# Kernel optimization log

Hardware: AMD Instinct MI355X
Metric: run time of the kernel (lower is better)

## Reference

```python
import jax, jax.numpy as jnp
import numpy as np

D_MODEL = 1024
NUM_HEADS = 16
D_K = D_MODEL // NUM_HEADS
NEG_INF = -1e9


def setup_inputs() -> dict:
    key = jax.random.key(0)
    ks = jax.random.split(key, 12)
    B, S = 2, 2048
    scale = 1.0 / np.sqrt(D_MODEL)
    inp = {
        "q": jax.random.normal(ks[0], (B, S, D_MODEL), jnp.float32),
        "k": jax.random.normal(ks[1], (B, S, D_MODEL), jnp.float32),
        "v": jax.random.normal(ks[2], (B, S, D_MODEL), jnp.float32),
        "mask": jnp.ones((B, S), jnp.int32),
        "W_q": jax.random.normal(ks[3], (D_MODEL, D_MODEL), jnp.float32) * scale,
        "b_q": jnp.zeros((D_MODEL,), jnp.float32),
        "W_k": jax.random.normal(ks[4], (D_MODEL, D_MODEL), jnp.float32) * scale,
        "b_k": jnp.zeros((D_MODEL,), jnp.float32),
        "W_v": jax.random.normal(ks[5], (D_MODEL, D_MODEL), jnp.float32) * scale,
        "b_v": jnp.zeros((D_MODEL,), jnp.float32),
        "W_o": jax.random.normal(ks[6], (D_MODEL, D_MODEL), jnp.float32) * scale,
        "b_o": jnp.zeros((D_MODEL,), jnp.float32),
    }
    return inp


def reference(q, k, v, mask, W_q, b_q, W_k, b_k, W_v, b_v, W_o, b_o):
    B, S, _ = q.shape
    def proj(x, W, b):
        # [B,S,D] -> [B,H,S,d_k]
        y = x @ W.T + b
        return y.reshape(B, -1, NUM_HEADS, D_K).transpose(0, 2, 1, 3)
    qh = proj(q, W_q, b_q)
    kh = proj(k, W_k, b_k)
    vh = proj(v, W_v, b_v)
    scores = jnp.einsum("bhqd,bhkd->bhqk", qh, kh) / jnp.sqrt(jnp.float32(D_K))
    # 2D mask [B,S_k] -> broadcast over heads and query positions
    m = mask[:, None, None, :]
    scores = jnp.where(m == 0, jnp.float32(NEG_INF), scores)
    attn = jax.nn.softmax(scores, axis=-1)
    # dropout is identity at inference
    context = jnp.einsum("bhqk,bhkd->bhqd", attn, vh)
    context = context.transpose(0, 2, 1, 3).reshape(B, S, D_MODEL)
    return context @ W_o.T + b_o
```

## Files before the change

kernel.cpp:

```cpp
#include <hip/hip_runtime.h>
#include <hip/hip_bf16.h>
#include <cstdint>
#include <cstddef>

#define DMODEL 1024
#define NHEADS 16
#define DK 64
#define SEQ 2048
#define BATCH 2
#define NT2 (SEQ / 64)

typedef short bf16x8 __attribute__((ext_vector_type(8)));
typedef float f32x4 __attribute__((ext_vector_type(4)));
typedef float f32x16 __attribute__((ext_vector_type(16)));
typedef unsigned int u32x2 __attribute__((ext_vector_type(2)));
typedef unsigned int u32x4 __attribute__((ext_vector_type(4)));

typedef const __attribute__((address_space(1))) void* gas_ptr;
typedef __attribute__((address_space(3))) void* las_ptr;

__device__ __forceinline__ void gld_lds16(const void* g, void* l) {
    __builtin_amdgcn_global_load_lds((gas_ptr)g, (las_ptr)l, 16, 0, 0);
}

__device__ __forceinline__ ushort f2bf_u(float f) {
    uint32_t x = __float_as_uint(f);
    x += 0x7fff + ((x >> 16) & 1);
    return (ushort)(x >> 16);
}

__global__ __launch_bounds__(256) void cast_all(
        const float* __restrict__ q, const float* __restrict__ k,
        const float* __restrict__ v, const float* __restrict__ Wq,
        const float* __restrict__ Wk, const float* __restrict__ Wv,
        const float* __restrict__ Wo,
        ushort* __restrict__ qb, ushort* __restrict__ kb, ushort* __restrict__ vb,
        ushort* __restrict__ Wqb, ushort* __restrict__ Wkb,
        ushort* __restrict__ Wvb, ushort* __restrict__ Wob) {
    int bid = blockIdx.x;
    const float* src; ushort* dst; int base;
    if      (bid <  4096) { src = q;  dst = qb;  base = bid; }
    else if (bid <  8192) { src = k;  dst = kb;  base = bid - 4096; }
    else if (bid < 12288) { src = v;  dst = vb;  base = bid - 8192; }
    else if (bid < 13312) { src = Wq; dst = Wqb; base = bid - 12288; }
    else if (bid < 14336) { src = Wk; dst = Wkb; base = bid - 13312; }
    else if (bid < 15360) { src = Wv; dst = Wvb; base = bid - 14336; }
    else                  { src = Wo; dst = Wob; base = bid - 15360; }
    int i = base * 1024 + threadIdx.x * 4;
    float4 f = *reinterpret_cast<const float4*>(src + i);
    ushort4 o;
    o.x = f2bf_u(f.x); o.y = f2bf_u(f.y); o.z = f2bf_u(f.z); o.w = f2bf_u(f.w);
    *reinterpret_cast<ushort4*>(dst + i) = o;
}

__global__ __launch_bounds__(256) void mask2bias(
        const int* __restrict__ m, float* __restrict__ mb) {
    int i = (blockIdx.x * 256 + threadIdx.x) * 4;
    int4 mk = *reinterpret_cast<const int4*>(m + i);
    float4 o;
    o.x = mk.x ? 0.f : -1e9f;
    o.y = mk.y ? 0.f : -1e9f;
    o.z = mk.z ? 0.f : -1e9f;
    o.w = mk.w ? 0.f : -1e9f;
    *reinterpret_cast<float4*>(mb + i) = o;
}

__global__ __launch_bounds__(256) void gemm_qkv(
        const ushort* __restrict__ A,
        const ushort* __restrict__ Wall,
        const float* __restrict__ bq, const float* __restrict__ bk,
        const float* __restrict__ bv,
        ushort* __restrict__ Qh, ushort* __restrict__ Kh, ushort* __restrict__ Vt) {
    __shared__ ushort As[128 * 32];
    __shared__ ushort Bs[128 * 32];
    const int tid = threadIdx.x;
    const int w = tid >> 6, lane = tid & 63;
    const int lr = lane & 15, lg = lane >> 4;
    int lid = (blockIdx.x & 7) * 96 + (blockIdx.x >> 3);
    const int tMg = (lid >> 3) << 7;
    const int tN  = (lid & 7) << 7;
    const int g   = tMg >> 12;
    const ushort* W = Wall + (size_t)g * 1024 * 1024;
    const float* bias = (g == 0) ? bq : (g == 1 ? bk : bv);
    const int wr = (w >> 1) * 64, wc = (w & 1) * 64;

    f32x4 acc[4][4] = {};

    const int c0 = (w * 2 + 0) * 64 + lane;
    const int c1 = (w * 2 + 1) * 64 + lane;
    const ushort* gA0 = A + (size_t)(tMg + (c0 >> 2)) * 1024 + (c0 & 3) * 8;
    const ushort* gA1 = A + (size_t)(tMg + (c1 >> 2)) * 1024 + (c1 & 3) * 8;
    const ushort* gB0 = W + (size_t)(tN + (c0 >> 2)) * 1024 + (c0 & 3) * 8;
    const ushort* gB1 = W + (size_t)(tN + (c1 >> 2)) * 1024 + (c1 & 3) * 8;
    ushort* lA0 = As + (w * 2 + 0) * 512;
    ushort* lA1 = As + (w * 2 + 1) * 512;
    ushort* lB0 = Bs + (w * 2 + 0) * 512;
    ushort* lB1 = Bs + (w * 2 + 1) * 512;

    for (int k0 = 0; k0 < 1024; k0 += 32) {
        gld_lds16(gA0 + k0, lA0);
        gld_lds16(gA1 + k0, lA1);
        gld_lds16(gB0 + k0, lB0);
        gld_lds16(gB1 + k0, lB1);
        __syncthreads();

        bf16x8 af[4], bfr[4];
#pragma unroll
        for (int i = 0; i < 4; i++)
            af[i] = *(const bf16x8*)(As + (wr + i * 16 + lr) * 32 + lg * 8);
#pragma unroll
        for (int i = 0; i < 4; i++)
            bfr[i] = *(const bf16x8*)(Bs + (wc + i * 16 + lr) * 32 + lg * 8);
#pragma unroll
        for (int mi = 0; mi < 4; mi++)
#pragma unroll
            for (int ni = 0; ni < 4; ni++)
                acc[mi][ni] = __builtin_amdgcn_mfma_f32_16x16x32_bf16(
                    af[mi], bfr[ni], acc[mi][ni], 0, 0, 0);
        __syncthreads();
    }

#pragma unroll
    for (int mi = 0; mi < 4; mi++) {
        const int row0 = tMg + wr + mi * 16 + lg * 4;
#pragma unroll
        for (int ni = 0; ni < 4; ni++) {
            const int col = tN + wc + ni * 16 + lr;
            const int h = col >> 6, d = col & (DK - 1);
            const float bvv = bias[col];
            if (g == 2) {
                int mloc = row0 & 4095;
                int b = mloc >> 11, s0 = mloc & (SEQ - 1);
                ushort4 o4;
                o4.x = f2bf_u(acc[mi][ni][0] + bvv);
                o4.y = f2bf_u(acc[mi][ni][1] + bvv);
                o4.z = f2bf_u(acc[mi][ni][2] + bvv);
                o4.w = f2bf_u(acc[mi][ni][3] + bvv);
                *reinterpret_cast<ushort4*>(
                    &Vt[(((size_t)(b * NHEADS + h) * DK + d) * SEQ) + s0]) = o4;
            } else {
#pragma unroll
                for (int r = 0; r < 4; r++) {
                    float vv = acc[mi][ni][r] + bvv;
                    int mloc = (row0 + r) & 4095;
                    int b = mloc >> 11, s = mloc & (SEQ - 1);
                    if (g == 0)
                        Qh[(((size_t)(b * NHEADS + h) * SEQ + s) * DK) + d] = f2bf_u(vv);
                    else
                        Kh[(((size_t)(b * NHEADS + h) * SEQ + s) * DK) + d] = f2bf_u(vv);
                }
            }
        }
    }
}

__global__ __launch_bounds__(256) void gemm_out(
        const ushort* __restrict__ A,
        const ushort* __restrict__ W,
        const float* __restrict__ bias,
        float* __restrict__ out, int M, int N, int K) {
    __shared__ ushort As[64 * 32];
    __shared__ ushort Bs[128 * 32];
    const int tid = threadIdx.x;
    const int w = tid >> 6, lane = tid & 63;
    const int lr = lane & 15, lg = lane >> 4;
    const int nTiles = N >> 7;
    const int cpx = gridDim.x >> 3;
    int lid = (blockIdx.x & 7) * cpx + (blockIdx.x >> 3);
    const int tM = (lid / nTiles) << 6;
    const int tN = (lid % nTiles) << 7;
    const int wr = (w >> 1) * 32, wc = (w & 1) * 64;

    f32x4 acc[2][4] = {};

    const int cA = w * 64 + lane;
    const int cB0 = w * 128 + lane;
    const int cB1 = w * 128 + 64 + lane;
    const ushort* gA  = A + (size_t)(tM + (cA  >> 2)) * K + (cA  & 3) * 8;
    const ushort* gB0 = W + (size_t)(tN + (cB0 >> 2)) * K + (cB0 & 3) * 8;
    const ushort* gB1 = W + (size_t)(tN + (cB1 >> 2)) * K + (cB1 & 3) * 8;
    ushort* lA  = As + w * 512;
    ushort* lB0 = Bs + w * 1024;
    ushort* lB1 = Bs + w * 1024 + 512;

    for (int k0 = 0; k0 < K; k0 += 32) {
        gld_lds16(gA  + k0, lA);
        gld_lds16(gB0 + k0, lB0);
        gld_lds16(gB1 + k0, lB1);
        __syncthreads();

        bf16x8 af[2], bfr[4];
#pragma unroll
        for (int i = 0; i < 2; i++)
            af[i] = *(const bf16x8*)(As + (wr + i * 16 + lr) * 32 + lg * 8);
#pragma unroll
        for (int i = 0; i < 4; i++)
            bfr[i] = *(const bf16x8*)(Bs + (wc + i * 16 + lr) * 32 + lg * 8);
#pragma unroll
        for (int mi = 0; mi < 2; mi++)
#pragma unroll
            for (int ni = 0; ni < 4; ni++)
                acc[mi][ni] = __builtin_amdgcn_mfma_f32_16x16x32_bf16(
                    af[mi], bfr[ni], acc[mi][ni], 0, 0, 0);
        __syncthreads();
    }

#pragma unroll
    for (int mi = 0; mi < 2; mi++) {
        const int row0 = tM + wr + mi * 16 + lg * 4;
#pragma unroll
        for (int ni = 0; ni < 4; ni++) {
            const int col = tN + wc + ni * 16 + lr;
            const float bv = bias[col];
#pragma unroll
            for (int r = 0; r < 4; r++)
                out[(size_t)(row0 + r) * N + col] = acc[mi][ni][r] + bv;
        }
    }
}

#define SCALE2 0.18033688011120542f

__device__ __forceinline__ bf16x8 pack_pa(const float* p) {
    uint a, b, c, d;
    asm("v_cvt_pk_bf16_f32 %0, %1, %2" : "=v"(a) : "v"(p[0]), "v"(p[1]));
    asm("v_cvt_pk_bf16_f32 %0, %1, %2" : "=v"(b) : "v"(p[4]), "v"(p[5]));
    asm("v_cvt_pk_bf16_f32 %0, %1, %2" : "=v"(c) : "v"(p[2]), "v"(p[3]));
    asm("v_cvt_pk_bf16_f32 %0, %1, %2" : "=v"(d) : "v"(p[6]), "v"(p[7]));
    asm("v_permlane32_swap_b32 %0, %1" : "+v"(a), "+v"(b));
    asm("v_permlane32_swap_b32 %0, %1" : "+v"(c), "+v"(d));
    union { u32x4 u; bf16x8 h; } cv;
    cv.u = (u32x4){a, c, b, d};
    return cv.h;
}

__device__ __forceinline__ float xadd32(float x) {
    u32x2 r = __builtin_amdgcn_permlane32_swap(__float_as_uint(x), __float_as_uint(x), false, false);
    return __uint_as_float(r[0]) + __uint_as_float(r[1]);
}

__device__ __forceinline__ float tsum16(const float* p) {
    float a0 = p[0] + p[1],   a1 = p[2] + p[3];
    float a2 = p[4] + p[5],   a3 = p[6] + p[7];
    float a4 = p[8] + p[9],   a5 = p[10] + p[11];
    float a6 = p[12] + p[13], a7 = p[14] + p[15];
    float b0 = a0 + a1, b1 = a2 + a3, b2 = a4 + a5, b3 = a6 + a7;
    return (b0 + b1) + (b2 + b3);
}

__global__ __launch_bounds__(256) void attn_fwd32(
        const ushort* __restrict__ Qh, const ushort* __restrict__ Kh,
        const ushort* __restrict__ Vt, const float* __restrict__ mbias,
        ushort* __restrict__ ctx) {
    __shared__ ushort Ks[2][2][2048];
    __shared__ ushort Vs[2][2][2048];
    __shared__ float  Ml[SEQ];

    const int tid = threadIdx.x;
    const int w = tid >> 6;
    const int l = tid & 63;
    const int q32 = l & 31, hi = l >> 5;
    const int q7 = l & 7;

    int lid = (blockIdx.x & 7) * 64 + (blockIdx.x >> 3);
    const int qblk = lid & 15;
    const int bh = lid >> 4;
    const int b = bh >> 4;
    const int h = bh & 15;
    const int q0 = qblk * 128 + w * 32;

    const ushort* Qp = Qh + (size_t)bh * SEQ * DK + (size_t)(q0 + q32) * DK + hi * 8;
    const ushort* Kg = Kh + (size_t)bh * SEQ * DK;
    const ushort* Vg = Vt + (size_t)bh * DK * SEQ;

    const int srow = tid >> 3;
    const int scs  = (tid & 7) ^ (srow & 7);
    const ushort* Ksrc = Kg + (size_t)srow * DK + scs * 8;
    const ushort* Vsrc = Vg + (size_t)(srow + ((scs & 4) << 3)) * SEQ + (scs & 3) * 8;

    {
        const float* mg = mbias + (size_t)b * SEQ;
        gld_lds16(mg + tid * 4,        &Ml[w * 256]);
        gld_lds16(mg + 1024 + tid * 4, &Ml[1024 + w * 256]);
    }

    auto STAGE = [&](int buf, int t) {
        const int kv0 = t * 64;
        gld_lds16(Ksrc + (size_t)kv0 * DK,        &Ks[buf][0][w * 512]);
        gld_lds16(Ksrc + (size_t)(kv0 + 32) * DK, &Ks[buf][1][w * 512]);
        gld_lds16(Vsrc + kv0,                     &Vs[buf][0][w * 512]);
        gld_lds16(Vsrc + kv0 + 32,                &Vs[buf][1][w * 512]);
    };

    bf16x8 qf[4];
#pragma unroll
    for (int dc = 0; dc < 4; dc++)
        qf[dc] = *(const bf16x8*)(Qp + dc * 16);

    f32x16 c0 = {}, c1 = {};
    float lrun = 0.f;

    STAGE(0, 0);
    __syncthreads();

    for (int t = 0; t < NT2; ++t) {
        const int buf = t & 1;
        if (t + 1 < NT2) STAGE(buf ^ 1, t + 1);

        const int kv0 = t * 64;

        bf16x8 kf0[4], kf1[4];
#pragma unroll
        for (int dc = 0; dc < 4; dc++)
            kf0[dc] = *(const bf16x8*)(&Ks[buf][0][q32 * 64 + (((dc * 2 + hi) ^ q7) * 8)]);
        f32x16 s0 = {}, s1 = {};
        __builtin_amdgcn_s_setprio(1);
#pragma unroll
        for (int dc = 0; dc < 4; dc++)
            s0 = __builtin_amdgcn_mfma_f32_32x32x16_bf16(kf0[dc], qf[dc], s0, 0, 0, 0);
        __builtin_amdgcn_s_setprio(0);
#pragma unroll
        for (int dc = 0; dc < 4; dc++)
            kf1[dc] = *(const bf16x8*)(&Ks[buf][1][q32 * 64 + (((dc * 2 + hi) ^ q7) * 8)]);
        __builtin_amdgcn_s_setprio(1);
#pragma unroll
        for (int dc = 0; dc < 4; dc++)
            s1 = __builtin_amdgcn_mfma_f32_32x32x16_bf16(kf1[dc], qf[dc], s1, 0, 0, 0);
        __builtin_amdgcn_s_setprio(0);

        float e0[16];
#pragma unroll
        for (int g = 0; g < 4; g++) {
            float4 mb0 = *reinterpret_cast<const float4*>(&Ml[kv0 + g * 8 + hi * 4]);
#pragma unroll
            for (int j = 0; j < 4; j++)
                e0[g * 4 + j] = __builtin_amdgcn_exp2f(
                    fmaf(s0[g * 4 + j], SCALE2, reinterpret_cast<const float*>(&mb0)[j]));
        }
        bf16x8 pa00 = pack_pa(e0);
        bf16x8 pa01 = pack_pa(e0 + 8);
        bf16x8 vc0[4];
#pragma unroll
        for (int dt = 0; dt < 2; dt++)
#pragma unroll
            for (int ks = 0; ks < 2; ks++)
                vc0[dt * 2 + ks] = *(const bf16x8*)(&Vs[buf][0][q32 * 64 + (((dt * 4 + ks * 2 + hi) ^ q7) * 8)]);
        __builtin_amdgcn_s_setprio(1);
        c0 = __builtin_amdgcn_mfma_f32_32x32x16_bf16(pa00, vc0[0], c0, 0, 0, 0);
        c1 = __builtin_amdgcn_mfma_f32_32x32x16_bf16(pa00, vc0[2], c1, 0, 0, 0);
        c0 = __builtin_amdgcn_mfma_f32_32x32x16_bf16(pa01, vc0[1], c0, 0, 0, 0);
        c1 = __builtin_amdgcn_mfma_f32_32x32x16_bf16(pa01, vc0[3], c1, 0, 0, 0);
        __builtin_amdgcn_s_setprio(0);
        lrun += tsum16(e0);

        float e1[16];
#pragma unroll
        for (int g = 0; g < 4; g++) {
            float4 mb1 = *reinterpret_cast<const float4*>(&Ml[kv0 + 32 + g * 8 + hi * 4]);
#pragma unroll
            for (int j = 0; j < 4; j++)
                e1[g * 4 + j] = __builtin_amdgcn_exp2f(
                    fmaf(s1[g * 4 + j], SCALE2, reinterpret_cast<const float*>(&mb1)[j]));
        }
        bf16x8 pa10 = pack_pa(e1);
        bf16x8 pa11 = pack_pa(e1 + 8);
        bf16x8 vc1[4];
#pragma unroll
        for (int dt = 0; dt < 2; dt++)
#pragma unroll
            for (int ks = 0; ks < 2; ks++)
                vc1[dt * 2 + ks] = *(const bf16x8*)(&Vs[buf][1][q32 * 64 + (((dt * 4 + ks * 2 + hi) ^ q7) * 8)]);
        __builtin_amdgcn_s_setprio(1);
        c0 = __builtin_amdgcn_mfma_f32_32x32x16_bf16(pa10, vc1[0], c0, 0, 0, 0);
        c1 = __builtin_amdgcn_mfma_f32_32x32x16_bf16(pa10, vc1[2], c1, 0, 0, 0);
        c0 = __builtin_amdgcn_mfma_f32_32x32x16_bf16(pa11, vc1[1], c0, 0, 0, 0);
        c1 = __builtin_amdgcn_mfma_f32_32x32x16_bf16(pa11, vc1[3], c1, 0, 0, 0);
        __builtin_amdgcn_s_setprio(0);
        lrun += tsum16(e1);

        __syncthreads();
    }

    float rl = 1.0f / xadd32(lrun);
#pragma unroll
    for (int r = 0; r < 16; r++) {
        int crow = (r & 3) + 8 * (r >> 2) + 4 * hi;
        float rlT = __shfl(rl, crow);
        int qq = q0 + crow;
        size_t base = (size_t)(b * SEQ + qq) * DMODEL + h * DK;
        ctx[base + q32]      = f2bf_u(c0[r] * rlT);
        ctx[base + 32 + q32] = f2bf_u(c1[r] * rlT);
    }
}

extern "C" void kernel_launch(void* const* d_in, const int* in_sizes, int n_in,
                              void* d_out, int out_size, void* d_ws, size_t ws_size,
                              hipStream_t stream) {
    const float* q    = (const float*)d_in[0];
    const float* k    = (const float*)d_in[1];
    const float* v    = (const float*)d_in[2];
    const int*   mask = (const int*)d_in[3];
    const float* Wq   = (const float*)d_in[4];
    const float* bq   = (const float*)d_in[5];
    const float* Wk   = (const float*)d_in[6];
    const float* bk   = (const float*)d_in[7];
    const float* Wv   = (const float*)d_in[8];
    const float* bv   = (const float*)d_in[9];
    const float* Wo   = (const float*)d_in[10];
    const float* bo   = (const float*)d_in[11];

    char* ws = (char*)d_ws;
    ushort* qb   = (ushort*)(ws + (size_t)0);
    ushort* kb   = (ushort*)(ws + ((size_t)8  << 20));
    ushort* vb   = (ushort*)(ws + ((size_t)16 << 20));
    ushort* Wqb  = (ushort*)(ws + ((size_t)24 << 20));
    ushort* Wkb  = (ushort*)(ws + ((size_t)26 << 20));
    ushort* Wvb  = (ushort*)(ws + ((size_t)28 << 20));
    ushort* Wob  = (ushort*)(ws + ((size_t)30 << 20));
    ushort* Qh   = (ushort*)(ws + ((size_t)32 << 20));
    ushort* Kh   = (ushort*)(ws + ((size_t)40 << 20));
    ushort* Vt   = (ushort*)(ws + ((size_t)48 << 20));
    ushort* ctxb = (ushort*)(ws + ((size_t)56 << 20));
    float*  mbias = (float*)(ws + (size_t)0);

    cast_all<<<16384, 256, 0, stream>>>(q, k, v, Wq, Wk, Wv, Wo,
                                        qb, kb, vb, Wqb, Wkb, Wvb, Wob);

    gemm_qkv<<<768, 256, 0, stream>>>(qb, Wqb, bq, bk, bv, Qh, Kh, Vt);

    mask2bias<<<BATCH * SEQ / 1024, 256, 0, stream>>>(mask, mbias);

    attn_fwd32<<<BATCH * NHEADS * (SEQ / 128), 256, 0, stream>>>(Qh, Kh, Vt, mbias, ctxb);

    const int M = BATCH * SEQ;
    gemm_out<<<(M / 64) * (DMODEL / 128), 256, 0, stream>>>(
        ctxb, Wob, bo, (float*)d_out, M, DMODEL, DMODEL);
}
```

Measured before the change: 142.6 us.

## Double GEMM K-tile to 64 and XOR-swizzle LDS layout in projection kernels

Both the QKV projection GEMM and the output projection GEMM now stage 64-wide K slices per iteration instead of 32. This halves the number of barrier pairs and loop iterations. The global-to-LDS loads permute 16-byte chunks with an XOR of the row index, and the fragment reads undo that permutation, to avoid LDS bank conflicts on the wider rows. LDS use per block doubles, which may reduce occupancy.

```diff
diff --git a/kernel.cpp b/kernel.cpp
--- a/kernel.cpp
+++ b/kernel.cpp
@@ -71,8 +71,8 @@
         const float* __restrict__ bq, const float* __restrict__ bk,
         const float* __restrict__ bv,
         ushort* __restrict__ Qh, ushort* __restrict__ Kh, ushort* __restrict__ Vt) {
-    __shared__ ushort As[128 * 32];
-    __shared__ ushort Bs[128 * 32];
+    __shared__ ushort As[128 * 64];
+    __shared__ ushort Bs[128 * 64];
     const int tid = threadIdx.x;
     const int w = tid >> 6, lane = tid & 63;
     const int lr = lane & 15, lg = lane >> 4;
@@ -86,37 +86,44 @@
 
     f32x4 acc[4][4] = {};
 
-    const int c0 = (w * 2 + 0) * 64 + lane;
-    const int c1 = (w * 2 + 1) * 64 + lane;
-    const ushort* gA0 = A + (size_t)(tMg + (c0 >> 2)) * 1024 + (c0 & 3) * 8;
-    const ushort* gA1 = A + (size_t)(tMg + (c1 >> 2)) * 1024 + (c1 & 3) * 8;
-    const ushort* gB0 = W + (size_t)(tN + (c0 >> 2)) * 1024 + (c0 & 3) * 8;
-    const ushort* gB1 = W + (size_t)(tN + (c1 >> 2)) * 1024 + (c1 & 3) * 8;
-    ushort* lA0 = As + (w * 2 + 0) * 512;
-    ushort* lA1 = As + (w * 2 + 1) * 512;
-    ushort* lB0 = Bs + (w * 2 + 0) * 512;
-    ushort* lB1 = Bs + (w * 2 + 1) * 512;
-
-    for (int k0 = 0; k0 < 1024; k0 += 32) {
-        gld_lds16(gA0 + k0, lA0);
-        gld_lds16(gA1 + k0, lA1);
-        gld_lds16(gB0 + k0, lB0);
-        gld_lds16(gB1 + k0, lB1);
+    const ushort* gAsrc[4];
+    const ushort* gBsrc[4];
+#pragma unroll
+    for (int i = 0; i < 4; i++) {
+        int slot = (w * 4 + i) * 64 + lane;
+        int row = slot >> 3, sr = slot & 7;
+        int cd = sr ^ (row & 7);
+        gAsrc[i] = A + (size_t)(tMg + row) * 1024 + cd * 8;
+        gBsrc[i] = W + (size_t)(tN + row) * 1024 + cd * 8;
+    }
+
+    for (int k0 = 0; k0 < 1024; k0 += 64) {
+#pragma unroll
+        for (int i = 0; i < 4; i++)
+            gld_lds16(gAsrc[i] + k0, As + (w * 4 + i) * 512);
+#pragma unroll
+        for (int i = 0; i < 4; i++)
+            gld_lds16(gBsrc[i] + k0, Bs + (w * 4 + i) * 512);
         __syncthreads();
 
-        bf16x8 af[4], bfr[4];
-#pragma unroll
-        for (int i = 0; i < 4; i++)
-            af[i] = *(const bf16x8*)(As + (wr + i * 16 + lr) * 32 + lg * 8);
-#pragma unroll
-        for (int i = 0; i < 4; i++)
-            bfr[i] = *(const bf16x8*)(Bs + (wc + i * 16 + lr) * 32 + lg * 8);
-#pragma unroll
-        for (int mi = 0; mi < 4; mi++)
-#pragma unroll
-            for (int ni = 0; ni < 4; ni++)
-                acc[mi][ni] = __builtin_amdgcn_mfma_f32_16x16x32_bf16(
-                    af[mi], bfr[ni], acc[mi][ni], 0, 0, 0);
+#pragma unroll
+        for (int ks = 0; ks < 2; ks++) {
+            bf16x8 af[4], bfr[4];
+#pragma unroll
+            for (int i = 0; i < 4; i++)
+                af[i] = *(const bf16x8*)(As + (wr + i * 16 + lr) * 64 +
+                                         (((ks * 4 + lg) ^ (lr & 7)) * 8));
+#pragma unroll
+            for (int i = 0; i < 4; i++)
+                bfr[i] = *(const bf16x8*)(Bs + (wc + i * 16 + lr) * 64 +
+                                          (((ks * 4 + lg) ^ (lr & 7)) * 8));
+#pragma unroll
+            for (int mi = 0; mi < 4; mi++)
+#pragma unroll
+                for (int ni = 0; ni < 4; ni++)
+                    acc[mi][ni] = __builtin_amdgcn_mfma_f32_16x16x32_bf16(
+                        af[mi], bfr[ni], acc[mi][ni], 0, 0, 0);
+        }
         __syncthreads();
     }
 
@@ -159,8 +166,8 @@
         const ushort* __restrict__ W,
         const float* __restrict__ bias,
         float* __restrict__ out, int M, int N, int K) {
-    __shared__ ushort As[64 * 32];
-    __shared__ ushort Bs[128 * 32];
+    __shared__ ushort As[64 * 64];
+    __shared__ ushort Bs[128 * 64];
     const int tid = threadIdx.x;
     const int w = tid >> 6, lane = tid & 63;
     const int lr = lane & 15, lg = lane >> 4;
@@ -173,35 +180,50 @@
 
     f32x4 acc[2][4] = {};
 
-    const int cA = w * 64 + lane;
-    const int cB0 = w * 128 + lane;
-    const int cB1 = w * 128 + 64 + lane;
-    const ushort* gA  = A + (size_t)(tM + (cA  >> 2)) * K + (cA  & 3) * 8;
-    const ushort* gB0 = W + (size_t)(tN + (cB0 >> 2)) * K + (cB0 & 3) * 8;
-    const ushort* gB1 = W + (size_t)(tN + (cB1 >> 2)) * K + (cB1 & 3) * 8;
-    ushort* lA  = As + w * 512;
-    ushort* lB0 = Bs + w * 1024;
-    ushort* lB1 = Bs + w * 1024 + 512;
-
-    for (int k0 = 0; k0 < K; k0 += 32) {
-        gld_lds16(gA  + k0, lA);
-        gld_lds16(gB0 + k0, lB0);
-        gld_lds16(gB1 + k0, lB1);
+    const ushort* gAsrc[2];
+    const ushort* gBsrc[4];
+#pragma unroll
+    for (int i = 0; i < 2; i++) {
+        int slot = (w * 2 + i) * 64 + lane;
+        int row = slot >> 3, sr = slot & 7;
+        int cd = sr ^ (row & 7);
+        gAsrc[i] = A + (size_t)(tM + row) * K + cd * 8;
+    }
+#pragma unroll
+    for (int i = 0; i < 4; i++) {
+        int slot = (w * 4 + i) * 64 + lane;
+        int row = slot >> 3, sr = slot & 7;
+        int cd = sr ^ (row & 7);
+        gBsrc[i] = W + (size_t)(tN + row) * K + cd * 8;
+    }
+
+    for (int k0 = 0; k0 < K; k0 += 64) {
+#pragma unroll
+        for (int i = 0; i < 2; i++)
+            gld_lds16(gAsrc[i] + k0, As + (w * 2 + i) * 512);
+#pragma unroll
+        for (int i = 0; i < 4; i++)
+            gld_lds16(gBsrc[i] + k0, Bs + (w * 4 + i) * 512);
         __syncthreads();
 
-        bf16x8 af[2], bfr[4];
-#pragma unroll
-        for (int i = 0; i < 2; i++)
-            af[i] = *(const bf16x8*)(As + (wr + i * 16 + lr) * 32 + lg * 8);
-#pragma unroll
-        for (int i = 0; i < 4; i++)
-            bfr[i] = *(const bf16x8*)(Bs + (wc + i * 16 + lr) * 32 + lg * 8);
-#pragma unroll
-        for (int mi = 0; mi < 2; mi++)
-#pragma unroll
-            for (int ni = 0; ni < 4; ni++)
-                acc[mi][ni] = __builtin_amdgcn_mfma_f32_16x16x32_bf16(
-                    af[mi], bfr[ni], acc[mi][ni], 0, 0, 0);
+#pragma unroll
+        for (int ks = 0; ks < 2; ks++) {
+            bf16x8 af[2], bfr[4];
+#pragma unroll
+            for (int i = 0; i < 2; i++)
+                af[i] = *(const bf16x8*)(As + (wr + i * 16 + lr) * 64 +
+                                         (((ks * 4 + lg) ^ (lr & 7)) * 8));
+#pragma unroll
+            for (int i = 0; i < 4; i++)
+                bfr[i] = *(const bf16x8*)(Bs + (wc + i * 16 + lr) * 64 +
+                                          (((ks * 4 + lg) ^ (lr & 7)) * 8));
+#pragma unroll
+            for (int mi = 0; mi < 2; mi++)
+#pragma unroll
+                for (int ni = 0; ni < 4; ni++)
+                    acc[mi][ni] = __builtin_amdgcn_mfma_f32_16x16x32_bf16(
+                        af[mi], bfr[ni], acc[mi][ni], 0, 0, 0);
+        }
         __syncthreads();
     }
 
```

Result: faster. 133.6 us (-6.3%).
